# Kernel optimization log

Hardware: AMD Instinct MI355X
Metric: run time of the kernel (lower is better)

## Reference

```python
import jax, jax.numpy as jnp
import numpy as np

N_HEAD, D_MODEL, D_HEAD = 16, 1024, 64
BSZ, QLEN, KLEN = 4, 1024, 2048
MEM_LEN = KLEN - QLEN


def _rel_shift(x):
    # x: [b, q, k, n] -> Transformer-XL relative shift
    b, q, k, n = x.shape
    zero_pad = jnp.zeros((b, q, 1, n), dtype=x.dtype)
    x_padded = jnp.concatenate([zero_pad, x], axis=2)        # [b, q, k+1, n]
    x_padded = x_padded.reshape(b, k + 1, q, n)
    return x_padded[:, 1:].reshape(b, q, k, n)


def setup_inputs() -> dict:
    key = jax.random.key(0)
    ks = jax.random.split(key, 8)
    s = 0.02
    w = jax.random.normal(ks[0], (BSZ, KLEN, D_MODEL), jnp.float32)
    r = jax.random.normal(ks[1], (1, KLEN, D_MODEL), jnp.float32)
    r_w_bias = jax.random.normal(ks[2], (N_HEAD, D_HEAD), jnp.float32) * s
    r_r_bias = jax.random.normal(ks[3], (N_HEAD, D_HEAD), jnp.float32) * s
    Wq = jax.random.normal(ks[4], (D_MODEL, N_HEAD * D_HEAD), jnp.float32) * s
    Wkv = jax.random.normal(ks[5], (D_MODEL, 2 * N_HEAD * D_HEAD), jnp.float32) * s
    Wr = jax.random.normal(ks[6], (D_MODEL, N_HEAD * D_HEAD), jnp.float32) * s
    Wo = jax.random.normal(ks[7], (N_HEAD * D_HEAD, D_MODEL), jnp.float32) * s
    # causal mask with memory: query i attends to j <= i + MEM_LEN
    attn_mask = jnp.triu(jnp.ones((QLEN, KLEN), dtype=bool), k=MEM_LEN + 1)
    return {"w": w, "r": r, "r_w_bias": r_w_bias, "r_r_bias": r_r_bias,
            "Wq": Wq, "Wkv": Wkv, "Wr": Wr, "Wo": Wo,
            "attn_mask": attn_mask, "qlen": QLEN}


def reference(w, r, r_w_bias, r_r_bias, Wq, Wkv, Wr, Wo, attn_mask, qlen):
    bsz, klen, _ = w.shape
    rlen = r.shape[1]
    scale = 1.0 / (D_HEAD ** 0.5)

    q = (w[:, -qlen:] @ Wq).reshape(bsz, qlen, N_HEAD, D_HEAD)
    kv = w @ Wkv
    k, v = jnp.split(kv, 2, axis=-1)
    k = k.reshape(bsz, klen, N_HEAD, D_HEAD)
    v = v.reshape(bsz, klen, N_HEAD, D_HEAD)
    rk = (r[0] @ Wr).reshape(rlen, N_HEAD, D_HEAD)

    AC = jnp.einsum('bind,bjnd->bijn', q + r_w_bias, k)
    BD = jnp.einsum('bind,jnd->bijn', q + r_r_bias, rk)
    attn_score = (AC + _rel_shift(BD)) * scale
    attn_score = jnp.where(attn_mask[None, :, :, None], jnp.float32(-1e30), attn_score)
    attn_prob = jax.nn.softmax(attn_score, axis=2)
    attn_vec = jnp.einsum('bijn,bjnd->bind', attn_prob, v)
    attn_vec = attn_vec.reshape(bsz, qlen, N_HEAD * D_HEAD)
    return attn_vec @ Wo
```

## Files before the change

### kernel.cpp

```cpp
#include <hip/hip_runtime.h>

constexpr int BSZ  = 4;
constexpr int NH   = 16;
constexpr int DH   = 64;
constexpr int QL   = 1024;
constexpr int KLN  = 2048;
constexpr int DM   = 1024;
constexpr int MEM  = 1024;

typedef __bf16 bf16x8  __attribute__((ext_vector_type(8)));
typedef __bf16 bf16x4t __attribute__((ext_vector_type(4)));
typedef float  f32x4   __attribute__((ext_vector_type(4)));

__device__ __forceinline__ void g2l16(__bf16* lds, const __bf16* g) {
    __builtin_amdgcn_global_load_lds(
        (const __attribute__((address_space(1))) unsigned int*)g,
        (__attribute__((address_space(3))) unsigned int*)lds, 16, 0, 0);
}

__global__ __launch_bounds__(256)
void prep(const float* __restrict__ w, const float* __restrict__ r,
          const float* __restrict__ Wq, const float* __restrict__ Wr,
          const float* __restrict__ Wo, const float* __restrict__ Wkv,
          __bf16* __restrict__ wbh, __bf16* __restrict__ rbh,
          __bf16* __restrict__ WqT, __bf16* __restrict__ WrT,
          __bf16* __restrict__ WoT, __bf16* __restrict__ WkvT)
{
    __shared__ __bf16 t[64 * 72];
    const int id = blockIdx.x;
    if (id < 5120) {
        const float* in; __bf16* out; size_t i;
        if (id < 4096) { in = w; out = wbh; i = ((size_t)id * 256 + threadIdx.x) * 8; }
        else { in = r; out = rbh; i = ((size_t)(id - 4096) * 256 + threadIdx.x) * 8; }
        float4 a = *(const float4*)(in + i);
        float4 b = *(const float4*)(in + i + 4);
        bf16x8 y = {(__bf16)a.x, (__bf16)a.y, (__bf16)a.z, (__bf16)a.w,
                    (__bf16)b.x, (__bf16)b.y, (__bf16)b.z, (__bf16)b.w};
        *(bf16x8*)(out + i) = y;
        return;
    }
    const int tt = id - 5120;
    const int z = tt >> 9, rem = tt & 511;
    const int xx = rem & 31, yy = rem >> 5;
    const float* in; __bf16* out; int N;
    if (z == 0)      { in = Wq;  out = WqT;  N = 1024; }
    else if (z == 1) { in = Wr;  out = WrT;  N = 1024; }
    else if (z == 2) { in = Wo;  out = WoT;  N = 1024; }
    else             { in = Wkv; out = WkvT; N = 2048; }
    if (xx * 64 >= N) return;
    const int n0 = xx * 64, k0 = yy * 64;
    const int row = threadIdx.x >> 2, seg = (threadIdx.x & 3) << 4;
    const float* src = in + (long)(k0 + row) * N + n0 + seg;
#pragma unroll
    for (int u = 0; u < 16; u += 4) {
        float4 x = *(const float4*)(src + u);
        t[(seg + u + 0) * 72 + row] = (__bf16)x.x;
        t[(seg + u + 1) * 72 + row] = (__bf16)x.y;
        t[(seg + u + 2) * 72 + row] = (__bf16)x.z;
        t[(seg + u + 3) * 72 + row] = (__bf16)x.w;
    }
    __syncthreads();
    __bf16* dst = out + (long)(n0 + row) * 1024 + k0 + seg;
    *(uint4*)(dst)     = *(const uint4*)(t + row * 72 + seg);
    *(uint4*)(dst + 8) = *(const uint4*)(t + row * 72 + seg + 8);
}

__device__ __forceinline__ void gemm_core(
    const __bf16* __restrict__ A, const __bf16* __restrict__ BT,
    __bf16* As, __bf16* Bs, int m0, int n0, int K, f32x4 (&acc)[4][4])
{
    const int tid = threadIdx.x, w = tid >> 6, l = tid & 63;
    const int il = l & 15, quad = l >> 4;
    const int wm = (w >> 1) * 64, wn = (w & 1) * 64;
    const int srow = l >> 3, scl = l & 7;

    const __bf16* ag = A  + (long)(m0 + w * 32 + srow) * K + ((scl ^ srow) << 3);
    const __bf16* bg = BT + (long)(n0 + w * 32 + srow) * K + ((scl ^ srow) << 3);
    const int xk0 = ((quad) ^ (il & 7)) << 3;
    const int xk1 = ((quad + 4) ^ (il & 7)) << 3;

#pragma unroll
    for (int j = 0; j < 4; ++j) {
        g2l16(As + (w * 32 + 8 * j) * 64, ag + (size_t)(8 * j) * K);
        g2l16(Bs + (w * 32 + 8 * j) * 64, bg + (size_t)(8 * j) * K);
    }
    __syncthreads();

    int cur = 0;
    for (int k0 = 0; k0 < K; k0 += 64) {
        const int nxt = cur ^ 1;
        if (k0 + 64 < K) {
#pragma unroll
            for (int j = 0; j < 4; ++j) {
                g2l16(As + nxt * 8192 + (w * 32 + 8 * j) * 64,
                      ag + k0 + 64 + (size_t)(8 * j) * K);
                g2l16(Bs + nxt * 8192 + (w * 32 + 8 * j) * 64,
                      bg + k0 + 64 + (size_t)(8 * j) * K);
            }
        }

        bf16x8 af[4][2], bf[4][2];
#pragma unroll
        for (int f = 0; f < 4; ++f) {
            const __bf16* ar = As + cur * 8192 + (wm + f * 16 + il) * 64;
            af[f][0] = *(const bf16x8*)(ar + xk0);
            af[f][1] = *(const bf16x8*)(ar + xk1);
            const __bf16* br = Bs + cur * 8192 + (wn + f * 16 + il) * 64;
            bf[f][0] = *(const bf16x8*)(br + xk0);
            bf[f][1] = *(const bf16x8*)(br + xk1);
        }
#pragma unroll
        for (int i = 0; i < 4; ++i)
#pragma unroll
            for (int j = 0; j < 4; ++j) {
                acc[i][j] = __builtin_amdgcn_mfma_f32_16x16x32_bf16(
                    af[i][0], bf[j][0], acc[i][j], 0, 0, 0);
                acc[i][j] = __builtin_amdgcn_mfma_f32_16x16x32_bf16(
                    af[i][1], bf[j][1], acc[i][j], 0, 0, 0);
            }

        __syncthreads();
        cur = nxt;
    }
}

__global__ __launch_bounds__(256, 2)
void gemm_proj(const __bf16* __restrict__ wbh, const __bf16* __restrict__ rbh,
               const __bf16* __restrict__ WqT, const __bf16* __restrict__ WkvT,
               const __bf16* __restrict__ WrT,
               __bf16* __restrict__ qwh, __bf16* __restrict__ qrh,
               __bf16* __restrict__ kh, __bf16* __restrict__ vhT,
               __bf16* __restrict__ rkh,
               const float* __restrict__ bw, const float* __restrict__ br)
{
    __shared__ __bf16 As[2 * 128 * 64];
    __shared__ __bf16 Bs[2 * 128 * 64];
    const int id = blockIdx.x;
    const __bf16 *A, *BT;
    int m0, n0, zz, kind;
    if (id < 1024) {
        n0 = (id & 15) * 128; m0 = ((id >> 4) & 15) * 128; zz = id >> 8;
        A = wbh + (size_t)zz * KLN * DM; BT = WkvT; kind = 3;
    } else if (id < 1280) {
        const int t = id - 1024;
        n0 = (t & 7) * 128; m0 = ((t >> 3) & 7) * 128; zz = t >> 6;
        A = wbh + (size_t)zz * KLN * DM + (size_t)MEM * DM; BT = WqT; kind = 2;
    } else {
        const int t = id - 1280;
        n0 = (t & 7) * 128; m0 = (t >> 3) * 128; zz = 0;
        A = rbh; BT = WrT; kind = 4;
    }

    f32x4 acc[4][4] = {};
    gemm_core(A, BT, As, Bs, m0, n0, DM, acc);

    const int tid = threadIdx.x, w = tid >> 6, l = tid & 63;
    const int il = l & 15, quad = l >> 4;
    const int wm = (w >> 1) * 64, wn = (w & 1) * 64;

    if (kind == 2) {
#pragma unroll
        for (int j = 0; j < 4; ++j) {
            const int col = n0 + wn + j * 16 + il;
            const int hn = col >> 6, d = col & 63;
            const float bwv = bw[col], brv = br[col];
            __bf16* q1 = qwh + ((size_t)(zz * 16 + hn) * 1024) * 64 + d;
            __bf16* q2 = qrh + ((size_t)(zz * 16 + hn) * 1024) * 64 + d;
#pragma unroll
            for (int i = 0; i < 4; ++i) {
                const int mb = m0 + wm + i * 16 + quad * 4;
#pragma unroll
                for (int rr = 0; rr < 4; ++rr) {
                    float v = acc[i][j][rr];
                    q1[(size_t)(mb + rr) * 64] = (__bf16)(v + bwv);
                    q2[(size_t)(mb + rr) * 64] = (__bf16)(v + brv);
                }
            }
        }
    } else if (kind == 3) {
        if (n0 + wn < 1024) {
#pragma unroll
            for (int j = 0; j < 4; ++j) {
                const int col = n0 + wn + j * 16 + il;
                const int hn = col >> 6, d = col & 63;
                __bf16* kp = kh + ((size_t)(zz * 16 + hn) * 2048) * 64 + d;
#pragma unroll
                for (int i = 0; i < 4; ++i) {
                    const int mb = m0 + wm + i * 16 + quad * 4;
#pragma unroll
                    for (int rr = 0; rr < 4; ++rr)
                        kp[(size_t)(mb + rr) * 64] = (__bf16)acc[i][j][rr];
                }
            }
        } else {
#pragma unroll
            for (int j = 0; j < 4; ++j) {
                const int col = n0 + wn + j * 16 + il - 1024;
                const int hn = col >> 6, d = col & 63;
                __bf16* vp = vhT + ((size_t)((zz * 16 + hn) * 64 + d)) * 2048;
#pragma unroll
                for (int i = 0; i < 4; ++i) {
                    const int mb = m0 + wm + i * 16 + quad * 4;
                    bf16x4t pk = {(__bf16)acc[i][j][0], (__bf16)acc[i][j][1],
                                  (__bf16)acc[i][j][2], (__bf16)acc[i][j][3]};
                    *(bf16x4t*)(vp + mb) = pk;
                }
            }
        }
    } else {
#pragma unroll
        for (int j = 0; j < 4; ++j) {
            const int col = n0 + wn + j * 16 + il;
            const int hn = col >> 6, d = col & 63;
            __bf16* rp = rkh + ((size_t)hn * 2048) * 64 + d;
#pragma unroll
            for (int i = 0; i < 4; ++i) {
                const int mb = m0 + wm + i * 16 + quad * 4;
#pragma unroll
                for (int rr = 0; rr < 4; ++rr)
                    rp[(size_t)(mb + rr) * 64] = (__bf16)acc[i][j][rr];
            }
        }
    }
}

__global__ __launch_bounds__(256, 2)
void gemm_out(const __bf16* __restrict__ avh, const __bf16* __restrict__ WoT,
              float* __restrict__ C)
{
    __shared__ __bf16 As[2 * 128 * 64];
    __shared__ __bf16 Bs[2 * 128 * 64];
    const int zz = blockIdx.z;
    const __bf16* A = avh + (size_t)zz * QL * DM;
    const int m0 = blockIdx.y * 128, n0 = blockIdx.x * 128;

    f32x4 acc[4][4] = {};
    gemm_core(A, WoT, As, Bs, m0, n0, DM, acc);

    const int tid = threadIdx.x, w = tid >> 6, l = tid & 63;
    const int il = l & 15, quad = l >> 4;
    const int wm = (w >> 1) * 64, wn = (w & 1) * 64;
    float* Cb = C + (size_t)zz * QL * DM;
#pragma unroll
    for (int i = 0; i < 4; ++i)
#pragma unroll
        for (int j = 0; j < 4; ++j) {
            float* cp = Cb + (long)(m0 + wm + i * 16 + quad * 4) * DM
                           + n0 + wn + j * 16 + il;
#pragma unroll
            for (int rr = 0; rr < 4; ++rr) cp[(long)rr * DM] = acc[i][j][rr];
        }
}

__global__ __launch_bounds__(256, 2)
void attn_mfma(const __bf16* __restrict__ qwh, const __bf16* __restrict__ qrh,
               const __bf16* __restrict__ kh, const __bf16* __restrict__ vhT,
               const __bf16* __restrict__ rkh, float* __restrict__ Op,
               float* __restrict__ ml)
{
    extern __shared__ __bf16 smem[];
    __bf16* kt  = smem;
    __bf16* vt  = smem + 4096;
    __bf16* rkt = smem + 8192;
    float*  scf = (float*)(smem + 20480);

    const int bx = blockIdx.x;
    const int part = bx & 1;
    const int bx2 = bx >> 1;
    const int ib = (bx2 & 1) ? (7 - (bx2 >> 1)) : (bx2 >> 1);
    const int i0 = ib * 128;
    const int n = blockIdx.y, b = blockIdx.z;
    const int tid = threadIdx.x;
    const int w = tid >> 6, l = tid & 63;
    const int il = l & 15, quad = l >> 4;
    const int iw0 = i0 + w * 32;

    bf16x8 qwf[2][2], qrf[2][2];
#pragma unroll
    for (int g = 0; g < 2; ++g) {
        const size_t qoff =
            ((size_t)((b * 16 + n) * QL + iw0 + 16 * g + il)) * 64 + quad * 8;
        qwf[g][0] = *(const bf16x8*)(qwh + qoff);
        qwf[g][1] = *(const bf16x8*)(qwh + qoff + 32);
        qrf[g][0] = *(const bf16x8*)(qrh + qoff);
        qrf[g][1] = *(const bf16x8*)(qrh + qoff + 32);
    }

    f32x4 O[2][4] = {};
    float m_i[2] = {-1e30f, -1e30f}, l_i[2] = {0.f, 0.f};
    const float c = 0.125f * 1.44269504f;

    const int srow = l >> 3, scl = l & 7;
    const __bf16* kbase  = kh  + ((size_t)((b * 16 + n) * KLN)) * 64;
    const __bf16* vbase0 = vhT + ((size_t)((b * 16 + n) * 64)) * KLN;
    const __bf16* rbp    = rkh + ((size_t)(n * KLN)) * 64;

    const int xk0 = ((quad) ^ (il & 7)) << 3;
    const int xk1 = ((quad + 4) ^ (il & 7)) << 3;

    const int nt = 2 * ib + 18;
    const int t0 = (part * nt) / 2;
    const int t1 = ((part + 1) * nt) / 2;
    int rot = (t0 % 3) * 64;

    const int ubB = 96 - 32 * w;

    for (int jt = t0; jt < t1; ++jt) {
        const int j0 = jt * 64;
        const int vu0 = j0 - i0 + 896;
        __syncthreads();
#pragma unroll
        for (int it = 0; it < 2; ++it) {
            const int row = w * 16 + it * 8 + srow;
            g2l16(kt + (w * 16 + it * 8) * 64,
                  kbase + ((size_t)(j0 + row)) * 64 + ((scl ^ srow) << 3));
        }
#pragma unroll
        for (int it = 0; it < 2; ++it) {
            const int row = w * 16 + it * 8 + srow;
            g2l16(vt + (w * 16 + it * 8) * 64,
                  vbase0 + (size_t)row * KLN + j0 + ((scl ^ srow) << 3));
        }
        if (jt == t0) {
#pragma unroll
            for (int it = 0; it < 6; ++it) {
                const int lbase = w * 48 + it * 8;
                int pb = lbase + rot; if (pb >= 192) pb -= 192;
                int vu = vu0 + lbase + srow;
                vu = vu < 0 ? 0 : (vu > KLN - 1 ? KLN - 1 : vu);
                g2l16(rkt + pb * 64,
                      rbp + (size_t)vu * 64 + ((scl ^ srow) << 3));
            }
        } else {
#pragma unroll
            for (int it = 0; it < 2; ++it) {
                const int lbase = 128 + w * 16 + it * 8;
                int pb = lbase + rot; if (pb >= 192) pb -= 192;
                int vu = vu0 + lbase + srow;
                vu = vu < 0 ? 0 : (vu > KLN - 1 ? KLN - 1 : vu);
                g2l16(rkt + pb * 64,
                      rbp + (size_t)vu * 64 + ((scl ^ srow) << 3));
            }
        }
        __syncthreads();

        const bool edge = (j0 + 63 > i0 + MEM);

        f32x4 sf[2][4];
#pragma unroll
        for (int fr = 0; fr < 4; ++fr) {
            const __bf16* ka = kt + (fr * 16 + il) * 64;
            bf16x8 a0 = *(const bf16x8*)(ka + xk0);
            bf16x8 a1 = *(const bf16x8*)(ka + xk1);
            __builtin_amdgcn_s_setprio(1);
#pragma unroll
            for (int g = 0; g < 2; ++g) {
                f32x4 acc = {};
                acc = __builtin_amdgcn_mfma_f32_16x16x32_bf16(a0, qwf[g][0], acc, 0, 0, 0);
                acc = __builtin_amdgcn_mfma_f32_16x16x32_bf16(a1, qwf[g][1], acc, 0, 0, 0);
                sf[g][fr] = acc;
            }
            __builtin_amdgcn_s_setprio(0);
        }

        bf16x8 ra[6][2];
#pragma unroll
        for (int uf2 = 0; uf2 < 6; ++uf2) {
            int pr = ubB + uf2 * 16 + il + rot; if (pr >= 192) pr -= 192;
            const __bf16* rp_ = rkt + pr * 64;
            ra[uf2][0] = *(const bf16x8*)(rp_ + xk0);
            ra[uf2][1] = *(const bf16x8*)(rp_ + xk1);
        }
        bf16x8 va[4][2];
#pragma unroll
        for (int df = 0; df < 4; ++df) {
            const __bf16* vp_ = vt + (df * 16 + il) * 64;
            va[df][0] = *(const bf16x8*)(vp_ + xk0);
            va[df][1] = *(const bf16x8*)(vp_ + xk1);
        }

        float* scw = scf + w * 1344;
#pragma unroll
        for (int g = 0; g < 2; ++g) {
#pragma unroll
            for (int uf = 0; uf < 5; ++uf) {
                const int idx = uf + 1 - g;
                f32x4 acc = {};
                __builtin_amdgcn_s_setprio(1);
                acc = __builtin_amdgcn_mfma_f32_16x16x32_bf16(ra[idx][0], qrf[g][0], acc, 0, 0, 0);
                acc = __builtin_amdgcn_mfma_f32_16x16x32_bf16(ra[idx][1], qrf[g][1], acc, 0, 0, 0);
                __builtin_amdgcn_s_setprio(0);
                *(f32x4*)(scw + il * 84 + uf * 16 + quad * 4) = acc;
            }

            const int i_gl = iw0 + 16 * g + il;
            float sv[4][4];
            float mfr[4];
#pragma unroll
            for (int fr = 0; fr < 4; ++fr) {
                const int base = il * 83 + fr * 16 + quad * 4 + 15;
#pragma unroll
                for (int rr = 0; rr < 4; ++rr) {
                    const int jl_ = fr * 16 + quad * 4 + rr;
                    float s = sf[g][fr][rr] + scw[base + rr];
                    if (edge) s = (j0 + jl_ > i_gl + MEM) ? -1e30f : s;
                    sv[fr][rr] = s;
                }
                mfr[fr] = fmaxf(fmaxf(sv[fr][0], sv[fr][1]),
                                fmaxf(sv[fr][2], sv[fr][3]));
            }
            const float tmax = fmaxf(fmaxf(mfr[0], mfr[1]),
                                     fmaxf(mfr[2], mfr[3]));
            if (!__all(tmax <= m_i[g] + 8.0f)) {
                float t2 = fmaxf(tmax, __shfl_xor(tmax, 16));
                t2 = fmaxf(t2, __shfl_xor(t2, 32));
                const float m_new = fmaxf(m_i[g], t2);
                const float alpha = exp2f((m_i[g] - m_new) * c);
                l_i[g] *= alpha;
#pragma unroll
                for (int df = 0; df < 4; ++df) O[g][df] *= alpha;
                m_i[g] = m_new;
            }
            const float m_cur = m_i[g];
            float pfr[4];
            __bf16* prow = (__bf16*)(scw + il * 84);
#pragma unroll
            for (int fr = 0; fr < 4; ++fr) {
                bf16x4t p4;
                float p0_ = exp2f((sv[fr][0] - m_cur) * c);
                float p1_ = exp2f((sv[fr][1] - m_cur) * c);
                float p2_ = exp2f((sv[fr][2] - m_cur) * c);
                float p3_ = exp2f((sv[fr][3] - m_cur) * c);
                p4[0] = (__bf16)p0_; p4[1] = (__bf16)p1_;
                p4[2] = (__bf16)p2_; p4[3] = (__bf16)p3_;
                pfr[fr] = (p0_ + p1_) + (p2_ + p3_);
                *(bf16x4t*)(prow + fr * 16 + quad * 4) = p4;
            }
            l_i[g] += (pfr[0] + pfr[1]) + (pfr[2] + pfr[3]);

            bf16x8 p0 = *(const bf16x8*)(prow + quad * 8);
            bf16x8 p1 = *(const bf16x8*)(prow + 32 + quad * 8);
            __builtin_amdgcn_s_setprio(1);
#pragma unroll
            for (int df = 0; df < 4; ++df) {
                O[g][df] = __builtin_amdgcn_mfma_f32_16x16x32_bf16(va[df][0], p0, O[g][df], 0, 0, 0);
                O[g][df] = __builtin_amdgcn_mfma_f32_16x16x32_bf16(va[df][1], p1, O[g][df], 0, 0, 0);
            }
            __builtin_amdgcn_s_setprio(0);
        }
        rot += 64; if (rot >= 192) rot -= 192;
    }

#pragma unroll
    for (int g = 0; g < 2; ++g) {
        l_i[g] += __shfl_xor(l_i[g], 16);
        l_i[g] += __shfl_xor(l_i[g], 32);
    }

#pragma unroll
    for (int g = 0; g < 2; ++g) {
        const int iL = w * 32 + 16 * g + il;
        float* opb = Op + (size_t)part * 4194304
                        + ((((size_t)b * NH + n) * 8 + ib)) * 8192
                        + (size_t)iL * 64 + quad * 4;
#pragma unroll
        for (int df = 0; df < 4; ++df)
            *(f32x4*)(opb + df * 16) = O[g][df];
        if (quad == 0) {
            const size_t base = (((size_t)b * NH + n) * 8 + ib) * 128 + iL;
            ml[(size_t)part * 65536 + base]          = m_i[g];
            ml[131072 + (size_t)part * 65536 + base] = l_i[g];
        }
    }
}

__global__ __launch_bounds__(256)
void attn_combine(const float* __restrict__ Op, const float* __restrict__ ml,
                  __bf16* __restrict__ av)
{
    const int tid = threadIdx.x;
    const int i = blockIdx.x * 4 + (tid >> 6);
    const int d = tid & 63;
    const int n = blockIdx.y, b = blockIdx.z;
    const int ib = i >> 7, iL = i & 127;
    const float c = 0.125f * 1.44269504f;

    const size_t mb = (((size_t)b * NH + n) * 8 + ib) * 128 + iL;
    const float m0 = ml[mb], m1 = ml[mb + 65536];
    const float l0 = ml[131072 + mb], l1 = ml[131072 + 65536 + mb];
    const float ms = fmaxf(m0, m1);
    const float w0 = exp2f((m0 - ms) * c);
    const float w1 = exp2f((m1 - ms) * c);
    const float ls = w0 * l0 + w1 * l1;

    const size_t ob = (((size_t)b * NH + n) * 8 + ib) * 8192
                      + (size_t)iL * 64 + d;
    const float o = w0 * Op[ob] + w1 * Op[ob + 4194304];
    av[((size_t)(b * QL + i)) * DM + n * 64 + d] = (__bf16)(o / ls);
}

extern "C" void kernel_launch(void* const* d_in, const int* in_sizes, int n_in,
                              void* d_out, int out_size, void* d_ws, size_t ws_size,
                              hipStream_t stream)
{
    const float* w   = (const float*)d_in[0];
    const float* r   = (const float*)d_in[1];
    const float* bwb = (const float*)d_in[2];
    const float* brb = (const float*)d_in[3];
    const float* Wq  = (const float*)d_in[4];
    const float* Wkv = (const float*)d_in[5];
    const float* Wr  = (const float*)d_in[6];
    const float* Wo  = (const float*)d_in[7];
    float* out = (float*)d_out;

    char* ws = (char*)d_ws;
    __bf16* wbh  = (__bf16*)(ws);
    __bf16* rbh  = (__bf16*)(ws + ((size_t)16 << 20));
    __bf16* WqT  = (__bf16*)(ws + ((size_t)20 << 20));
    __bf16* WkvT = (__bf16*)(ws + ((size_t)22 << 20));
    __bf16* WrT  = (__bf16*)(ws + ((size_t)26 << 20));
    __bf16* WoT  = (__bf16*)(ws + ((size_t)28 << 20));
    __bf16* qwh  = (__bf16*)(ws + ((size_t)30 << 20));
    __bf16* qrh  = (__bf16*)(ws + ((size_t)38 << 20));
    __bf16* kh   = (__bf16*)(ws + ((size_t)46 << 20));
    __bf16* vhT  = (__bf16*)(ws + ((size_t)62 << 20));
    __bf16* rkh  = (__bf16*)(ws + ((size_t)78 << 20));
    __bf16* avh  = (__bf16*)(ws + ((size_t)82 << 20));
    float*  Op   = (float*)(ws + ((size_t)90 << 20));
    float*  mlb  = (float*)(ws + ((size_t)122 << 20));

    dim3 blk(256);
    prep<<<7168, blk, 0, stream>>>(w, r, Wq, Wr, Wo, Wkv,
                                   wbh, rbh, WqT, WrT, WoT, WkvT);
    gemm_proj<<<1408, blk, 0, stream>>>(wbh, rbh, WqT, WkvT, WrT,
                                        qwh, qrh, kh, vhT, rkh, bwb, brb);
    attn_mfma<<<dim3(16, 16, 4), blk, 62464, stream>>>(
        qwh, qrh, kh, vhT, rkh, Op, mlb);
    attn_combine<<<dim3(256, 16, 4), blk, 0, stream>>>(Op, mlb, avh);
    gemm_out<<<dim3(8, 8, 4), blk, 0, stream>>>(avh, WoT, out);
}
```

Measured before the change: 330.6 us.

## Drop split-KV attention partitioning and normalize output directly in attention kernel

Removes the two-way split of the key range per query block, so each block processes all key tiles itself and writes normalized bf16 output straight into the attention-vector buffer. This eliminates the fp32 partial-output and max/sum writes plus the separate combine kernel launch. In exchange the grid halves to 512 blocks with longer, more imbalanced per-block work, which may reduce occupancy and parallelism on a large GPU.

```diff
diff --git a/kernel.cpp b/kernel.cpp
--- a/kernel.cpp
+++ b/kernel.cpp
@@ -255,8 +255,7 @@
 __global__ __launch_bounds__(256, 2)
 void attn_mfma(const __bf16* __restrict__ qwh, const __bf16* __restrict__ qrh,
                const __bf16* __restrict__ kh, const __bf16* __restrict__ vhT,
-               const __bf16* __restrict__ rkh, float* __restrict__ Op,
-               float* __restrict__ ml)
+               const __bf16* __restrict__ rkh, __bf16* __restrict__ av)
 {
     extern __shared__ __bf16 smem[];
     __bf16* kt  = smem;
@@ -265,9 +264,7 @@
     float*  scf = (float*)(smem + 20480);
 
     const int bx = blockIdx.x;
-    const int part = bx & 1;
-    const int bx2 = bx >> 1;
-    const int ib = (bx2 & 1) ? (7 - (bx2 >> 1)) : (bx2 >> 1);
+    const int ib = (bx & 1) ? (7 - (bx >> 1)) : (bx >> 1);
     const int i0 = ib * 128;
     const int n = blockIdx.y, b = blockIdx.z;
     const int tid = threadIdx.x;
@@ -299,13 +296,11 @@
     const int xk1 = ((quad + 4) ^ (il & 7)) << 3;
 
     const int nt = 2 * ib + 18;
-    const int t0 = (part * nt) / 2;
-    const int t1 = ((part + 1) * nt) / 2;
-    int rot = (t0 % 3) * 64;
+    int rot = 0;
 
     const int ubB = 96 - 32 * w;
 
-    for (int jt = t0; jt < t1; ++jt) {
+    for (int jt = 0; jt < nt; ++jt) {
         const int j0 = jt * 64;
         const int vu0 = j0 - i0 + 896;
         __syncthreads();
@@ -321,7 +316,7 @@
             g2l16(vt + (w * 16 + it * 8) * 64,
                   vbase0 + (size_t)row * KLN + j0 + ((scl ^ srow) << 3));
         }
-        if (jt == t0) {
+        if (jt == 0) {
 #pragma unroll
             for (int it = 0; it < 6; ++it) {
                 const int lbase = w * 48 + it * 8;
@@ -459,44 +454,16 @@
 
 #pragma unroll
     for (int g = 0; g < 2; ++g) {
-        const int iL = w * 32 + 16 * g + il;
-        float* opb = Op + (size_t)part * 4194304
-                        + ((((size_t)b * NH + n) * 8 + ib)) * 8192
-                        + (size_t)iL * 64 + quad * 4;
-#pragma unroll
-        for (int df = 0; df < 4; ++df)
-            *(f32x4*)(opb + df * 16) = O[g][df];
-        if (quad == 0) {
-            const size_t base = (((size_t)b * NH + n) * 8 + ib) * 128 + iL;
-            ml[(size_t)part * 65536 + base]          = m_i[g];
-            ml[131072 + (size_t)part * 65536 + base] = l_i[g];
-        }
-    }
-}
-
-__global__ __launch_bounds__(256)
-void attn_combine(const float* __restrict__ Op, const float* __restrict__ ml,
-                  __bf16* __restrict__ av)
-{
-    const int tid = threadIdx.x;
-    const int i = blockIdx.x * 4 + (tid >> 6);
-    const int d = tid & 63;
-    const int n = blockIdx.y, b = blockIdx.z;
-    const int ib = i >> 7, iL = i & 127;
-    const float c = 0.125f * 1.44269504f;
-
-    const size_t mb = (((size_t)b * NH + n) * 8 + ib) * 128 + iL;
-    const float m0 = ml[mb], m1 = ml[mb + 65536];
-    const float l0 = ml[131072 + mb], l1 = ml[131072 + 65536 + mb];
-    const float ms = fmaxf(m0, m1);
-    const float w0 = exp2f((m0 - ms) * c);
-    const float w1 = exp2f((m1 - ms) * c);
-    const float ls = w0 * l0 + w1 * l1;
-
-    const size_t ob = (((size_t)b * NH + n) * 8 + ib) * 8192
-                      + (size_t)iL * 64 + d;
-    const float o = w0 * Op[ob] + w1 * Op[ob + 4194304];
-    av[((size_t)(b * QL + i)) * DM + n * 64 + d] = (__bf16)(o / ls);
+        const float rl = 1.0f / l_i[g];
+        const int i_gl = i0 + w * 32 + 16 * g + il;
+        __bf16* avb = av + ((size_t)(b * QL + i_gl)) * DM + n * 64 + quad * 4;
+#pragma unroll
+        for (int df = 0; df < 4; ++df) {
+            bf16x4t o4 = {(__bf16)(O[g][df][0] * rl), (__bf16)(O[g][df][1] * rl),
+                          (__bf16)(O[g][df][2] * rl), (__bf16)(O[g][df][3] * rl)};
+            *(bf16x4t*)(avb + df * 16) = o4;
+        }
+    }
 }
 
 extern "C" void kernel_launch(void* const* d_in, const int* in_sizes, int n_in,
@@ -526,16 +493,13 @@
     __bf16* vhT  = (__bf16*)(ws + ((size_t)62 << 20));
     __bf16* rkh  = (__bf16*)(ws + ((size_t)78 << 20));
     __bf16* avh  = (__bf16*)(ws + ((size_t)82 << 20));
-    float*  Op   = (float*)(ws + ((size_t)90 << 20));
-    float*  mlb  = (float*)(ws + ((size_t)122 << 20));
 
     dim3 blk(256);
     prep<<<7168, blk, 0, stream>>>(w, r, Wq, Wr, Wo, Wkv,
                                    wbh, rbh, WqT, WrT, WoT, WkvT);
     gemm_proj<<<1408, blk, 0, stream>>>(wbh, rbh, WqT, WkvT, WrT,
                                         qwh, qrh, kh, vhT, rkh, bwb, brb);
-    attn_mfma<<<dim3(16, 16, 4), blk, 62464, stream>>>(
-        qwh, qrh, kh, vhT, rkh, Op, mlb);
-    attn_combine<<<dim3(256, 16, 4), blk, 0, stream>>>(Op, mlb, avh);
+    attn_mfma<<<dim3(8, 16, 4), blk, 62464, stream>>>(
+        qwh, qrh, kh, vhT, rkh, avh);
     gemm_out<<<dim3(8, 8, 4), blk, 0, stream>>>(avh, WoT, out);
 }
```

Result: faster. 313.4 us (-5.2%).
